# Performance work log

Hardware: AMD Instinct MI355X
Metric: run time of the kernel (lower is better)

The kernel has to match this reference:

```python
import jax, jax.numpy as jnp
import numpy as np

B, N, M = 32, 32, 64          # batch, timesteps, local group length (group_token_length+3)
NL, NG = 192, 768             # n_embd_local, n_embd_global
HL, HG = 6, 12                # n_head_local, n_head_global


def setup_inputs() -> dict:
    key = jax.random.key(0)
    ks = jax.random.split(key, 16)
    def w(k, shape, s=0.02):
        return jax.random.normal(k, shape, jnp.float32) * s
    inp = {}
    inp["xl"] = jax.random.normal(ks[0], (B, N, M, NL), jnp.float32)
    inp["xg"] = jax.random.normal(ks[1], (B, 2 * N, NG), jnp.float32)
    i = 2
    for pre, d in (("l", NL), ("g", NG)):
        inp[f"{pre}_ln1_w"] = jnp.ones((d,), jnp.float32)
        inp[f"{pre}_ln1_b"] = jnp.zeros((d,), jnp.float32)
        inp[f"{pre}_ln2_w"] = jnp.ones((d,), jnp.float32)
        inp[f"{pre}_ln2_b"] = jnp.zeros((d,), jnp.float32)
        for nm in ("q", "k", "v", "o"):
            inp[f"{pre}_w{nm}"] = w(ks[i], (d, d)); i += 1
            inp[f"{pre}_b{nm}"] = jnp.zeros((d,), jnp.float32)
        inp[f"{pre}_w1"] = w(ks[i], (d, 4 * d)); i += 1
        inp[f"{pre}_b1"] = jnp.zeros((4 * d,), jnp.float32)
        inp[f"{pre}_w2"] = w(ks[i], (4 * d, d)); i += 1
        inp[f"{pre}_b2"] = jnp.zeros((d,), jnp.float32)
    inp["d_w"] = w(ks[i], (M * NL, NG))
    inp["d_b"] = jnp.zeros((NG,), jnp.float32)
    return inp


def _ln(x, g, b):
    m = x.mean(-1, keepdims=True)
    v = ((x - m) ** 2).mean(-1, keepdims=True)
    return (x - m) / jnp.sqrt(v + 1e-5) * g + b


def _attn(x, wq, bq, wk, bk, wv, bv, wo, bo, nh, allow):
    # x: [B', L, D]; allow: [L, L] bool (True = attend)
    Bx, L, D = x.shape
    hd = D // nh
    q = (x @ wq + bq).reshape(Bx, L, nh, hd)
    k = (x @ wk + bk).reshape(Bx, L, nh, hd)
    v = (x @ wv + bv).reshape(Bx, L, nh, hd)
    s = jnp.einsum('bihd,bjhd->bhij', q, k) / np.float32(np.sqrt(hd))
    s = jnp.where(allow[None, None], s, -jnp.inf)
    p = jax.nn.softmax(s, axis=-1)
    y = jnp.einsum('bhij,bjhd->bihd', p, v).reshape(Bx, L, D)
    return y @ wo + bo


def _tblock(x, p, nh, allow):
    (ln1w, ln1b, ln2w, ln2b, wq, bq, wk, bk, wv, bv, wo, bo, w1, b1, w2, b2) = p
    x = x + _attn(_ln(x, ln1w, ln1b), wq, bq, wk, bk, wv, bv, wo, bo, nh, allow)
    h = _ln(x, ln2w, ln2b)
    return x + (jax.nn.gelu(h @ w1 + b1, approximate=False) @ w2 + b2)


def reference(xl, xg,
              l_ln1_w, l_ln1_b, l_ln2_w, l_ln2_b,
              l_wq, l_bq, l_wk, l_bk, l_wv, l_bv, l_wo, l_bo,
              l_w1, l_b1, l_w2, l_b2,
              g_ln1_w, g_ln1_b, g_ln2_w, g_ln2_b,
              g_wq, g_bq, g_wk, g_bk, g_wv, g_bv, g_wo, g_bo,
              g_w1, g_b1, g_w2, g_b2,
              d_w, d_b):
    Bx, Nx, Mx, nl = xl.shape
    ng = xg.shape[-1]
    lp = (l_ln1_w, l_ln1_b, l_ln2_w, l_ln2_b, l_wq, l_bq, l_wk, l_bk,
          l_wv, l_bv, l_wo, l_bo, l_w1, l_b1, l_w2, l_b2)
    gp = (g_ln1_w, g_ln1_b, g_ln2_w, g_ln2_b, g_wq, g_bq, g_wk, g_bk,
          g_wv, g_bv, g_wo, g_bo, g_w1, g_b1, g_w2, g_b2)

    # local block: causal attention within each group of M tokens
    allow_l = jnp.tril(jnp.ones((Mx, Mx), bool))
    x = _tblock(xl.reshape(Bx * Nx, Mx, nl), lp, HL, allow_l)
    xl_out = x.reshape(Bx, Nx, Mx, nl)

    # summarize each group into one global token, interleave with xg pairs
    zg = (xl_out.reshape(Bx, Nx, Mx * nl) @ d_w + d_b)[:, :, None, :]  # [B,N,1,ng]
    zg = jnp.concatenate([zg, xg.reshape(Bx, Nx, 2, ng)], axis=2)      # [B,N,3,ng]
    zg = zg.reshape(Bx, 3 * Nx, ng)

    # global mask: tril plus within-triplet upper entries; the global block
    # additionally applies its own causal mask, so combined = causal & custom
    L = 3 * Nx
    idx = jnp.arange(L)
    causal = idx[:, None] >= idx[None, :]
    custom = causal | (idx[:, None] // 3 == idx[None, :] // 3)
    allow_g = causal & custom

    zg = _tblock(zg, gp, HG, allow_g)
    xg_out = zg.reshape(Bx, Nx, 3, ng)[:, :, 1:, :].reshape(Bx, 2 * Nx, ng)
    return (xl_out, xg_out)
```

## Files before the change

kernel.cpp:

```cpp
#include <hip/hip_runtime.h>
#include <hip/hip_bf16.h>


typedef unsigned short ushort;
typedef __bf16 bf16x8 __attribute__((ext_vector_type(8)));
typedef float f32x4 __attribute__((ext_vector_type(4)));

__device__ __forceinline__ ushort f2us(float f) {
  __hip_bfloat16 h = __float2bfloat16(f);
  return *reinterpret_cast<ushort*>(&h);
}
__device__ __forceinline__ float gelu_exact(float v) {
  return 0.5f * v * (1.f + erff(v * 0.70710678118654752f));
}
__device__ __forceinline__ void gload16(const ushort* g, ushort* l) {
  __builtin_amdgcn_global_load_lds(
      (const __attribute__((address_space(1))) void*)g,
      (__attribute__((address_space(3))) void*)l, 16, 0, 0);
}

struct TJobs { const float* s[13]; ushort* d[13]; };

__global__ __launch_bounds__(256)
void transp_all(TJobs J)
{
  static constexpr int NN[13]  = {192,192,192,192,768,192,768,768,768,768,768,3072,768};
  static constexpr int SS[13]  = {192,192,192,192,192,768,12288,768,768,768,768,768,3072};
  static constexpr int RO[13]  = {0,192,384,0,0,0,0,0,768,1536,0,0,0};
  static constexpr int CUM[14] = {0,9,18,27,36,72,108,2412,2556,2700,2844,2988,3564,4140};
  __shared__ float t[64][65];
  int bid = blockIdx.x;
  int j = 0;
  while (bid >= CUM[j + 1]) ++j;
  int tIdx = bid - CUM[j];
  const int N = NN[j], stride = SS[j], rowOff = RO[j];
  const int nx = N >> 6;
  const int n0 = (tIdx % nx) * 64, k0 = (tIdx / nx) * 64;
  const float* W = J.s[j];
  ushort* Wt = J.d[j];
  int c = threadIdx.x & 63, r = threadIdx.x >> 6;
  #pragma unroll
  for (int i = 0; i < 16; ++i) {
    int kr = r + i * 4;
    t[kr][c] = W[(size_t)(k0 + kr) * N + n0 + c];
  }
  __syncthreads();
  #pragma unroll
  for (int i = 0; i < 16; ++i) {
    int nr = r + i * 4;
    Wt[(size_t)(rowOff + n0 + nr) * stride + k0 + c] = f2us(t[c][nr]);
  }
}

__global__ __launch_bounds__(256)
void pack3_kernel(float* dst, const float* a, int na, const float* b, int nb,
                  const float* c, int nc)
{
  int i = blockIdx.x * 256 + threadIdx.x;
  if (i >= na + nb + nc) return;
  dst[i] = (i < na) ? a[i] : (i < na + nb ? b[i - na] : c[i - na - nb]);
}

template<int D>
__global__ __launch_bounds__(256)
void ln_kernel(const float* __restrict__ x, const float* __restrict__ g,
               const float* __restrict__ bb, ushort* __restrict__ out, int rows)
{
  int wave = threadIdx.x >> 6, lane = threadIdx.x & 63;
  int row = blockIdx.x * 4 + wave;
  if (row >= rows) return;
  const float* xr = x + (size_t)row * D;
  constexpr int E = D / 64;
  float vals[E];
  float s = 0.f;
  #pragma unroll
  for (int e = 0; e < E; ++e) { vals[e] = xr[e * 64 + lane]; s += vals[e]; }
  #pragma unroll
  for (int off = 32; off >= 1; off >>= 1) s += __shfl_xor(s, off);
  float m = s * (1.f / D);
  float s2 = 0.f;
  #pragma unroll
  for (int e = 0; e < E; ++e) { float d = vals[e] - m; s2 += d * d; }
  #pragma unroll
  for (int off = 32; off >= 1; off >>= 1) s2 += __shfl_xor(s2, off);
  float rstd = rsqrtf(s2 * (1.f / D) + 1e-5f);
  ushort* orow = out + (size_t)row * D;
  #pragma unroll
  for (int e = 0; e < E; ++e) {
    int c = e * 64 + lane;
    orow[c] = f2us((vals[e] - m) * rstd * g[c] + bb[c]);
  }
}

template<int ACT, int RES, int OUTF, int OUTB, int BIAS>
__global__ __launch_bounds__(256)
void mgemm(const ushort* __restrict__ A, const ushort* __restrict__ Bt,
           const float* __restrict__ bias, const float* __restrict__ resF,
           float* __restrict__ Cf, ushort* __restrict__ Cb,
           int M, int N, int K)
{
  __shared__ __align__(16) ushort Asm[2][128 * 32];
  __shared__ __align__(16) ushort Bsm[2][64 * 32];
  const int tid = threadIdx.x;
  const int wave = tid >> 6, lane = tid & 63;
  const int quad = lane >> 4, lm = lane & 15;
  const int rowBase = blockIdx.y * 128, colBase = blockIdx.x * 64;
  const int wrow = (wave & 1) * 64, wcol = (wave >> 1) * 32;
  const int srow = lane >> 2, skcol = (lane & 3) * 8;
  const int nIter = K >> 5;

  auto stage = [&](int buf, int it) {
    const int k0 = it * 32;
    #pragma unroll
    for (int uu = 0; uu < 3; ++uu) {
      const int u = wave * 3 + uu;
      if (u < 8) {
        const ushort* gp = A + (size_t)(rowBase + u * 16 + srow) * K + k0 + skcol;
        gload16(gp, &Asm[buf][u * 512]);
      } else {
        const int v = u - 8;
        const ushort* gp = Bt + (size_t)(colBase + v * 16 + srow) * K + k0 + skcol;
        gload16(gp, &Bsm[buf][v * 512]);
      }
    }
  };

  f32x4 acc[4][2] = {};
  stage(0, 0);
  if (nIter > 1) stage(1, 1);

  for (int t = 0; t < nIter; ++t) {
    const int cur = t & 1;
    if (t + 1 < nIter) asm volatile("s_waitcnt vmcnt(3)" ::: "memory");
    else               asm volatile("s_waitcnt vmcnt(0)" ::: "memory");
    __builtin_amdgcn_s_barrier();
    bf16x8 af[4], bfr[2];
    #pragma unroll
    for (int r2 = 0; r2 < 4; ++r2)
      af[r2] = *reinterpret_cast<const bf16x8*>(&Asm[cur][(wrow + r2 * 16 + lm) * 32 + quad * 8]);
    #pragma unroll
    for (int c2 = 0; c2 < 2; ++c2)
      bfr[c2] = *reinterpret_cast<const bf16x8*>(&Bsm[cur][(wcol + c2 * 16 + lm) * 32 + quad * 8]);
    asm volatile("s_waitcnt lgkmcnt(0)" ::: "memory");
    __builtin_amdgcn_s_barrier();
    if (t + 2 < nIter) stage(cur, t + 2);
    #pragma unroll
    for (int r2 = 0; r2 < 4; ++r2)
      #pragma unroll
      for (int c2 = 0; c2 < 2; ++c2)
        acc[r2][c2] = __builtin_amdgcn_mfma_f32_16x16x32_bf16(af[r2], bfr[c2], acc[r2][c2], 0, 0, 0);
  }

  #pragma unroll
  for (int r2 = 0; r2 < 4; ++r2) {
    #pragma unroll
    for (int c2 = 0; c2 < 2; ++c2) {
      int col = colBase + wcol + c2 * 16 + lm;
      int row0 = rowBase + wrow + r2 * 16 + quad * 4;
      #pragma unroll
      for (int g = 0; g < 4; ++g) {
        float v = acc[r2][c2][g];
        size_t idx = (size_t)(row0 + g) * N + col;
        if (BIAS) v += bias[col];
        if (ACT == 1) v = gelu_exact(v);
        if (RES) v += resF[idx];
        if (OUTF) Cf[idx] = v;
        if (OUTB) Cb[idx] = f2us(v);
      }
    }
  }
}

template<int ACT, int RES, int OUTF, int OUTB, int BIAS, int SPLITK>
__global__ __launch_bounds__(256)
void mgemm128(const ushort* __restrict__ A, const ushort* __restrict__ Bt,
              const float* __restrict__ bias, const float* __restrict__ resF,
              float* __restrict__ Cf, ushort* __restrict__ Cb,
              int M, int N, int K, int kChunk)
{
  __shared__ __align__(16) ushort Asm[2][128 * 32];
  __shared__ __align__(16) ushort Bsm[2][128 * 32];
  const int tid = threadIdx.x;
  const int wave = tid >> 6, lane = tid & 63;
  const int quad = lane >> 4, lm = lane & 15;
  const int rowBase = blockIdx.y * 128, colBase = blockIdx.x * 128;
  const int wrow = (wave & 1) * 64, wcol = (wave >> 1) * 64;
  const int srow = lane >> 2, skcol = (lane & 3) * 8;

  const int kbeg = SPLITK ? blockIdx.z * kChunk : 0;
  const int nIter = (SPLITK ? kChunk : K) >> 5;

  auto stage = [&](int buf, int it) {
    const int k0 = kbeg + it * 32;
    #pragma unroll
    for (int uu = 0; uu < 4; ++uu) {
      const int u = wave * 4 + uu;
      if (u < 8) {
        const ushort* gp = A + (size_t)(rowBase + u * 16 + srow) * K + k0 + skcol;
        gload16(gp, &Asm[buf][u * 512]);
      } else {
        const int v = u - 8;
        const ushort* gp = Bt + (size_t)(colBase + v * 16 + srow) * K + k0 + skcol;
        gload16(gp, &Bsm[buf][v * 512]);
      }
    }
  };

  f32x4 acc[4][4] = {};
  stage(0, 0);
  if (nIter > 1) stage(1, 1);

  for (int t = 0; t < nIter; ++t) {
    const int cur = t & 1;
    if (t + 1 < nIter) asm volatile("s_waitcnt vmcnt(4)" ::: "memory");
    else               asm volatile("s_waitcnt vmcnt(0)" ::: "memory");
    __builtin_amdgcn_s_barrier();
    bf16x8 af[4], bfr[4];
    #pragma unroll
    for (int r2 = 0; r2 < 4; ++r2)
      af[r2] = *reinterpret_cast<const bf16x8*>(&Asm[cur][(wrow + r2 * 16 + lm) * 32 + quad * 8]);
    #pragma unroll
    for (int c2 = 0; c2 < 4; ++c2)
      bfr[c2] = *reinterpret_cast<const bf16x8*>(&Bsm[cur][(wcol + c2 * 16 + lm) * 32 + quad * 8]);
    asm volatile("s_waitcnt lgkmcnt(0)" ::: "memory");
    __builtin_amdgcn_s_barrier();
    if (t + 2 < nIter) stage(cur, t + 2);
    #pragma unroll
    for (int r2 = 0; r2 < 4; ++r2)
      #pragma unroll
      for (int c2 = 0; c2 < 4; ++c2)
        acc[r2][c2] = __builtin_amdgcn_mfma_f32_16x16x32_bf16(af[r2], bfr[c2], acc[r2][c2], 0, 0, 0);
  }

  const size_t zoff = SPLITK ? (size_t)blockIdx.z * M * N : 0;
  #pragma unroll
  for (int r2 = 0; r2 < 4; ++r2) {
    #pragma unroll
    for (int c2 = 0; c2 < 4; ++c2) {
      int col = colBase + wcol + c2 * 16 + lm;
      int row0 = rowBase + wrow + r2 * 16 + quad * 4;
      #pragma unroll
      for (int g = 0; g < 4; ++g) {
        float v = acc[r2][c2][g];
        size_t idx = (size_t)(row0 + g) * N + col;
        if (BIAS) v += bias[col];
        if (ACT == 1) v = gelu_exact(v);
        if (RES) v += resF[idx];
        if (OUTF) Cf[zoff + idx] = v;
        if (OUTB) Cb[idx] = f2us(v);
      }
    }
  }
}

__global__ __launch_bounds__(256)
void reduce8_kernel(const float* __restrict__ P, const float* __restrict__ db,
                    float* __restrict__ ZG)
{
  int i = blockIdx.x * 256 + threadIdx.x;
  float s = db[i % 768];
  #pragma unroll
  for (int k = 0; k < 8; ++k) s += P[i + k * 786432];
  ZG[i] = s;
}

__global__ __launch_bounds__(256)
void reduce4res_kernel(const float* __restrict__ P, const float* __restrict__ db,
                       const float* __restrict__ res, float* __restrict__ out)
{
  int i = blockIdx.x * 256 + threadIdx.x;
  float s = db[i % 768] + res[i];
  #pragma unroll
  for (int k = 0; k < 4; ++k) s += P[i + k * 2359296];
  out[i] = s;
}

template<int L, int HD, int NW>
__global__ __launch_bounds__(NW * 64)
void fattn(const ushort* __restrict__ QKV, ushort* __restrict__ Yp,
           int nh, int DS, int DY, int offQ, int offK, int offV)
{
  constexpr int PQ = HD + 8;
  constexpr int PV = L + 8;
  constexpr int KS = HD / 32;
  constexpr int NCT = L / 16;
  constexpr int KS2 = L / 32;
  constexpr int NYT = HD / 16;
  constexpr int T = NW * 64;
  __shared__ __align__(16) ushort Ql[L * PQ];
  __shared__ __align__(16) ushort Kl[L * PQ];
  __shared__ __align__(16) ushort Vt[HD * PV];
  __shared__ __align__(16) ushort Ps[L * PV];
  const int tid = threadIdx.x;
  const int b = blockIdx.x / nh, h = blockIdx.x % nh;
  const size_t rowb = (size_t)b * L * DS;
  const int hb = h * HD;
  constexpr int CH = L * HD / 8;
  for (int idx = tid; idx < CH; idx += T) {
    int row = idx / (HD / 8), seg = idx % (HD / 8);
    uint4 q4 = *reinterpret_cast<const uint4*>(&QKV[rowb + (size_t)row * DS + offQ + hb + seg * 8]);
    *reinterpret_cast<uint4*>(&Ql[row * PQ + seg * 8]) = q4;
    uint4 k4 = *reinterpret_cast<const uint4*>(&QKV[rowb + (size_t)row * DS + offK + hb + seg * 8]);
    *reinterpret_cast<uint4*>(&Kl[row * PQ + seg * 8]) = k4;
  }
  for (int idx = tid; idx < L * HD; idx += T) {
    int j = idx / HD, d = idx % HD;
    Vt[d * PV + j] = QKV[rowb + (size_t)j * DS + offV + hb + d];
  }
  __syncthreads();
  const int lane = tid & 63;
  const int quad = lane >> 4, lm = lane & 15;
  const int rt = tid >> 6;
  const float scale = rsqrtf((float)HD);
  bf16x8 af[KS];
  #pragma unroll
  for (int s = 0; s < KS; ++s)
    af[s] = *reinterpret_cast<const bf16x8*>(&Ql[(rt * 16 + lm) * PQ + s * 32 + quad * 8]);
  f32x4 sacc[NCT] = {};
  #pragma unroll
  for (int ct = 0; ct < NCT; ++ct)
    #pragma unroll
    for (int s = 0; s < KS; ++s) {
      bf16x8 bf = *reinterpret_cast<const bf16x8*>(&Kl[(ct * 16 + lm) * PQ + s * 32 + quad * 8]);
      sacc[ct] = __builtin_amdgcn_mfma_f32_16x16x32_bf16(af[s], bf, sacc[ct], 0, 0, 0);
    }
  float inv[4];
  #pragma unroll
  for (int g = 0; g < 4; ++g) {
    const int row = rt * 16 + quad * 4 + g;
    float sv[NCT]; float m = -1e30f;
    #pragma unroll
    for (int ct = 0; ct < NCT; ++ct) {
      int col = ct * 16 + lm;
      float x = sacc[ct][g] * scale;
      sv[ct] = (col <= row) ? x : -1e30f;
      m = fmaxf(m, sv[ct]);
    }
    #pragma unroll
    for (int off = 8; off >= 1; off >>= 1) m = fmaxf(m, __shfl_xor(m, off));
    float l = 0.f;
    #pragma unroll
    for (int ct = 0; ct < NCT; ++ct) {
      float p = __expf(sv[ct] - m);
      l += p;
      Ps[row * PV + ct * 16 + lm] = f2us(p);
    }
    #pragma unroll
    for (int off = 8; off >= 1; off >>= 1) l += __shfl_xor(l, off);
    inv[g] = 1.f / l;
  }
  __syncthreads();
  f32x4 yacc[NYT] = {};
  #pragma unroll
  for (int s = 0; s < KS2; ++s) {
    bf16x8 ap = *reinterpret_cast<const bf16x8*>(&Ps[(rt * 16 + lm) * PV + s * 32 + quad * 8]);
    #pragma unroll
    for (int ct = 0; ct < NYT; ++ct) {
      bf16x8 bv = *reinterpret_cast<const bf16x8*>(&Vt[(ct * 16 + lm) * PV + s * 32 + quad * 8]);
      yacc[ct] = __builtin_amdgcn_mfma_f32_16x16x32_bf16(ap, bv, yacc[ct], 0, 0, 0);
    }
  }
  #pragma unroll
  for (int ct = 0; ct < NYT; ++ct)
    #pragma unroll
    for (int g = 0; g < 4; ++g) {
      int row = rt * 16 + quad * 4 + g;
      int d = ct * 16 + lm;
      Yp[((size_t)b * L + row) * DY + hb + d] = f2us(yacc[ct][g] * inv[g]);
    }
}

__global__ __launch_bounds__(256)
void interleave_kernel(const float* __restrict__ zg, const float* __restrict__ xg,
                       float* __restrict__ z)
{
  int idx = blockIdx.x * 256 + threadIdx.x;
  int c = idx % 768;
  int tok = idx / 768;
  int b = tok / 96, r = tok % 96;
  int n = r / 3, t = r % 3;
  z[idx] = (t == 0) ? zg[((size_t)b * 32 + n) * 768 + c]
                    : xg[((size_t)b * 64 + 2 * n + (t - 1)) * 768 + c];
}

__global__ __launch_bounds__(256)
void gather_kernel(const float* __restrict__ zfin, float* __restrict__ dst)
{
  int idx = blockIdx.x * 256 + threadIdx.x;
  int c = idx % 768;
  int t = (idx / 768) % 64;
  int b = idx / (768 * 64);
  int n = t >> 1, s = t & 1;
  dst[idx] = zfin[((size_t)b * 96 + 3 * n + 1 + s) * 768 + c];
}

extern "C" void kernel_launch(void* const* d_in, const int* in_sizes, int n_in,
                              void* d_out, int out_size, void* d_ws, size_t ws_size,
                              hipStream_t stream) {
  const float* xl = (const float*)d_in[0];
  const float* xg = (const float*)d_in[1];
  const float* l_ln1_w = (const float*)d_in[2];  const float* l_ln1_b = (const float*)d_in[3];
  const float* l_ln2_w = (const float*)d_in[4];  const float* l_ln2_b = (const float*)d_in[5];
  const float* l_wq = (const float*)d_in[6];     const float* l_bq = (const float*)d_in[7];
  const float* l_wk = (const float*)d_in[8];     const float* l_bk = (const float*)d_in[9];
  const float* l_wv = (const float*)d_in[10];    const float* l_bv = (const float*)d_in[11];
  const float* l_wo = (const float*)d_in[12];    const float* l_bo = (const float*)d_in[13];
  const float* l_w1 = (const float*)d_in[14];    const float* l_b1 = (const float*)d_in[15];
  const float* l_w2 = (const float*)d_in[16];    const float* l_b2 = (const float*)d_in[17];
  const float* g_ln1_w = (const float*)d_in[18]; const float* g_ln1_b = (const float*)d_in[19];
  const float* g_ln2_w = (const float*)d_in[20]; const float* g_ln2_b = (const float*)d_in[21];
  const float* g_wq = (const float*)d_in[22];    const float* g_bq = (const float*)d_in[23];
  const float* g_wk = (const float*)d_in[24];    const float* g_bk = (const float*)d_in[25];
  const float* g_wv = (const float*)d_in[26];    const float* g_bv = (const float*)d_in[27];
  const float* g_wo = (const float*)d_in[28];    const float* g_bo = (const float*)d_in[29];
  const float* g_w1 = (const float*)d_in[30];    const float* g_b1 = (const float*)d_in[31];
  const float* g_w2 = (const float*)d_in[32];    const float* g_b2 = (const float*)d_in[33];
  const float* dw   = (const float*)d_in[34];    const float* db   = (const float*)d_in[35];

  float* outL = (float*)d_out;
  float* outG = outL + 12582912;

  char* W = (char*)d_ws;
  ushort* A_bf   = (ushort*)(W + 0);
  ushort* QKVl   = (ushort*)(W + 25165824);
  ushort* HIDl   = (ushort*)(W + 25165824);
  ushort* XLb    = (ushort*)(W + 75497472);
  float*  X1     = (float*)(W + 100663296);
  ushort* wqkv_t = (ushort*)(W + 150994944);
  ushort* wo_t   = (ushort*)(W + 151216128);
  ushort* w1_t   = (ushort*)(W + 151289856);
  ushort* w2_t   = (ushort*)(W + 151584768);
  ushort* wd_t   = (ushort*)(W + 151879680);
  ushort* wgqkv_t= (ushort*)(W + 170754048);
  ushort* wgo_t  = (ushort*)(W + 174292992);
  ushort* wg1_t  = (ushort*)(W + 175472640);
  ushort* wg2_t  = (ushort*)(W + 180191232);
  float*  bqkv_l = (float*)(W + 184909824);
  float*  bqkv_g = (float*)(W + 184912128);
  float*  ZGP  = (float*)(W + 0);
  float*  FC2P = (float*)(W + 0);
  float*  ZG   = (float*)(W + 25165824);
  float*  Z    = (float*)(W + 28311552);
  ushort* LNG  = (ushort*)(W + 37748736);
  ushort* QKVg = (ushort*)(W + 42467328);
  ushort* YG   = (ushort*)(W + 56623104);
  float*  X1G  = (float*)(W + 61341696);
  ushort* HLNG = (ushort*)(W + 70778880);
  ushort* HIDg = (ushort*)(W + 100663296);
  float*  OUTG = (float*)(W + 119537664);

  TJobs tj;
  tj.s[0] = l_wq; tj.s[1] = l_wk; tj.s[2] = l_wv; tj.s[3] = l_wo;
  tj.s[4] = l_w1; tj.s[5] = l_w2; tj.s[6] = dw;
  tj.s[7] = g_wq; tj.s[8] = g_wk; tj.s[9] = g_wv; tj.s[10] = g_wo;
  tj.s[11] = g_w1; tj.s[12] = g_w2;
  tj.d[0] = wqkv_t; tj.d[1] = wqkv_t; tj.d[2] = wqkv_t; tj.d[3] = wo_t;
  tj.d[4] = w1_t; tj.d[5] = w2_t; tj.d[6] = wd_t;
  tj.d[7] = wgqkv_t; tj.d[8] = wgqkv_t; tj.d[9] = wgqkv_t; tj.d[10] = wgo_t;
  tj.d[11] = wg1_t; tj.d[12] = wg2_t;
  transp_all<<<4140, 256, 0, stream>>>(tj);
  pack3_kernel<<<3, 256, 0, stream>>>(bqkv_l, l_bq, 192, l_bk, 192, l_bv, 192);
  pack3_kernel<<<9, 256, 0, stream>>>(bqkv_g, g_bq, 768, g_bk, 768, g_bv, 768);

  ln_kernel<192><<<16384, 256, 0, stream>>>(xl, l_ln1_w, l_ln1_b, A_bf, 65536);
  mgemm<0,0,0,1,1><<<dim3(9,512), 256, 0, stream>>>(A_bf, wqkv_t, bqkv_l, nullptr, nullptr, QKVl, 65536, 576, 192);
  fattn<64,32,4><<<6144, 256, 0, stream>>>(QKVl, A_bf, 6, 576, 192, 0, 192, 384);
  mgemm<0,1,1,0,1><<<dim3(3,512), 256, 0, stream>>>(A_bf, wo_t, l_bo, xl, X1, nullptr, 65536, 192, 192);
  ln_kernel<192><<<16384, 256, 0, stream>>>(X1, l_ln2_w, l_ln2_b, A_bf, 65536);
  for (int h = 0; h < 2; ++h) {
    size_t ro = (size_t)h * 32768 * 192;
    mgemm128<1,0,0,1,1,0><<<dim3(6,256), 256, 0, stream>>>(A_bf + ro, w1_t, l_b1, nullptr, nullptr, HIDl, 32768, 768, 192, 0);
    mgemm<0,1,1,1,1><<<dim3(3,256), 256, 0, stream>>>(HIDl, w2_t, l_b2, X1 + ro, outL + ro, XLb + ro, 32768, 192, 768);
  }
  mgemm128<0,0,1,0,0,1><<<dim3(6,8,8), 256, 0, stream>>>(XLb, wd_t, nullptr, nullptr, ZGP, nullptr, 1024, 768, 12288, 1536);
  reduce8_kernel<<<3072, 256, 0, stream>>>(ZGP, db, ZG);
  interleave_kernel<<<9216, 256, 0, stream>>>(ZG, xg, Z);
  ln_kernel<768><<<768, 256, 0, stream>>>(Z, g_ln1_w, g_ln1_b, LNG, 3072);
  mgemm128<0,0,0,1,1,0><<<dim3(18,24), 256, 0, stream>>>(LNG, wgqkv_t, bqkv_g, nullptr, nullptr, QKVg, 3072, 2304, 768, 0);
  fattn<96,64,6><<<384, 384, 0, stream>>>(QKVg, YG, 12, 2304, 768, 0, 768, 1536);
  mgemm<0,1,1,0,1><<<dim3(12,24), 256, 0, stream>>>(YG, wgo_t, g_bo, Z, X1G, nullptr, 3072, 768, 768);
  ln_kernel<768><<<768, 256, 0, stream>>>(X1G, g_ln2_w, g_ln2_b, HLNG, 3072);
  mgemm128<1,0,0,1,1,0><<<dim3(24,24), 256, 0, stream>>>(HLNG, wg1_t, g_b1, nullptr, nullptr, HIDg, 3072, 3072, 768, 0);
  mgemm128<0,0,1,0,0,1><<<dim3(6,24,4), 256, 0, stream>>>(HIDg, wg2_t, nullptr, nullptr, FC2P, nullptr, 3072, 768, 3072, 768);
  reduce4res_kernel<<<9216, 256, 0, stream>>>(FC2P, g_b2, X1G, OUTG);
  gather_kernel<<<6144, 256, 0, stream>>>(OUTG, outG);
}
```

Before: 660.3 us.

## Fuse local MLP FC1+GELU+FC2 into one kernel keeping hidden in LDS

Replaces the two-pass local MLP (FC1 GEMM writing a bf16 hidden buffer, then FC2 GEMM with residual) with a single kernel. Each block owns 64 rows, computes the hidden activations 64 columns at a time into shared memory, and accumulates FC2 in registers, streaming W1/W2 tiles through registers into LDS. This removes the global write and re-read of the 65536x768 hidden tensor and several launches. In exchange it has lower per-block parallelism (1024 blocks, high register use for acc and A fragments) and frequent syncs per hidden tile.

```diff
diff --git a/kernel.cpp b/kernel.cpp
--- a/kernel.cpp
+++ b/kernel.cpp
@@ -90,6 +90,142 @@
     int c = e * 64 + lane;
     orow[c] = f2us((vals[e] - m) * rstd * g[c] + bb[c]);
   }
+}
+
+__global__ __launch_bounds__(256)
+void fused_mlp(const ushort* __restrict__ A, const ushort* __restrict__ W1t,
+               const ushort* __restrict__ W2t, const float* __restrict__ b1,
+               const float* __restrict__ b2, const float* __restrict__ resF,
+               float* __restrict__ Cf, ushort* __restrict__ Cb)
+{
+  __shared__ __align__(16) ushort W1B[64 * 200];
+  __shared__ __align__(16) ushort W2B[192 * 72];
+  __shared__ __align__(16) ushort Hs[64 * 72];
+  const int tid = threadIdx.x;
+  const int wave = tid >> 6, lane = tid & 63;
+  const int quad = lane >> 4, lm = lane & 15;
+  const int rowBase = blockIdx.x * 64;
+  const int wr  = (wave & 1) * 32;
+  const int wc1 = (wave >> 1) * 32;
+  const int wc2 = (wave >> 1) * 96;
+
+  bf16x8 afr[2][6];
+  #pragma unroll
+  for (int r2 = 0; r2 < 2; ++r2)
+    #pragma unroll
+    for (int kt = 0; kt < 6; ++kt)
+      afr[r2][kt] = *reinterpret_cast<const bf16x8*>(
+          &A[(size_t)(rowBase + wr + r2 * 16 + lm) * 192 + kt * 32 + quad * 8]);
+
+  uint4 rs1[6], rs2[6];
+  #pragma unroll
+  for (int i = 0; i < 6; ++i) {
+    int seg = tid + i * 256, row = seg / 24, kk = (seg % 24) * 8;
+    rs1[i] = *reinterpret_cast<const uint4*>(&W1t[(size_t)row * 192 + kk]);
+  }
+  #pragma unroll
+  for (int i = 0; i < 6; ++i) {
+    int seg = tid + i * 256, row = seg / 24, kk = (seg % 24) * 8;
+    *reinterpret_cast<uint4*>(&W1B[row * 200 + kk]) = rs1[i];
+  }
+  #pragma unroll
+  for (int i = 0; i < 6; ++i) {
+    int seg = tid + i * 256, row = seg / 8, kk = (seg % 8) * 8;
+    rs2[i] = *reinterpret_cast<const uint4*>(&W2t[(size_t)row * 768 + kk]);
+  }
+  __syncthreads();
+
+  f32x4 acc2[2][6] = {};
+  for (int ht = 0; ht < 12; ++ht) {
+    f32x4 acc1[2][2] = {};
+    #pragma unroll
+    for (int kt = 0; kt < 6; ++kt) {
+      bf16x8 bfr[2];
+      #pragma unroll
+      for (int c2 = 0; c2 < 2; ++c2)
+        bfr[c2] = *reinterpret_cast<const bf16x8*>(
+            &W1B[(wc1 + c2 * 16 + lm) * 200 + kt * 32 + quad * 8]);
+      #pragma unroll
+      for (int r2 = 0; r2 < 2; ++r2)
+        #pragma unroll
+        for (int c2 = 0; c2 < 2; ++c2)
+          acc1[r2][c2] = __builtin_amdgcn_mfma_f32_16x16x32_bf16(
+              afr[r2][kt], bfr[c2], acc1[r2][c2], 0, 0, 0);
+    }
+    #pragma unroll
+    for (int r2 = 0; r2 < 2; ++r2)
+      #pragma unroll
+      for (int c2 = 0; c2 < 2; ++c2) {
+        int col = wc1 + c2 * 16 + lm;
+        float bb1 = b1[ht * 64 + col];
+        #pragma unroll
+        for (int g = 0; g < 4; ++g) {
+          int row = wr + r2 * 16 + quad * 4 + g;
+          Hs[row * 72 + col] = f2us(gelu_exact(acc1[r2][c2][g] + bb1));
+        }
+      }
+    #pragma unroll
+    for (int i = 0; i < 6; ++i) {
+      int seg = tid + i * 256, row = seg / 8, kk = (seg % 8) * 8;
+      *reinterpret_cast<uint4*>(&W2B[row * 72 + kk]) = rs2[i];
+    }
+    if (ht + 1 < 12) {
+      #pragma unroll
+      for (int i = 0; i < 6; ++i) {
+        int seg = tid + i * 256, row = seg / 24, kk = (seg % 24) * 8;
+        rs1[i] = *reinterpret_cast<const uint4*>(
+            &W1t[(size_t)((ht + 1) * 64 + row) * 192 + kk]);
+      }
+    }
+    __syncthreads();
+    #pragma unroll
+    for (int s = 0; s < 2; ++s) {
+      bf16x8 ap[2], bp[6];
+      #pragma unroll
+      for (int r2 = 0; r2 < 2; ++r2)
+        ap[r2] = *reinterpret_cast<const bf16x8*>(
+            &Hs[(wr + r2 * 16 + lm) * 72 + s * 32 + quad * 8]);
+      #pragma unroll
+      for (int c2 = 0; c2 < 6; ++c2)
+        bp[c2] = *reinterpret_cast<const bf16x8*>(
+            &W2B[(wc2 + c2 * 16 + lm) * 72 + s * 32 + quad * 8]);
+      #pragma unroll
+      for (int r2 = 0; r2 < 2; ++r2)
+        #pragma unroll
+        for (int c2 = 0; c2 < 6; ++c2)
+          acc2[r2][c2] = __builtin_amdgcn_mfma_f32_16x16x32_bf16(
+              ap[r2], bp[c2], acc2[r2][c2], 0, 0, 0);
+    }
+    if (ht + 1 < 12) {
+      #pragma unroll
+      for (int i = 0; i < 6; ++i) {
+        int seg = tid + i * 256, row = seg / 24, kk = (seg % 24) * 8;
+        *reinterpret_cast<uint4*>(&W1B[row * 200 + kk]) = rs1[i];
+      }
+      #pragma unroll
+      for (int i = 0; i < 6; ++i) {
+        int seg = tid + i * 256, row = seg / 8, kk = (seg % 8) * 8;
+        rs2[i] = *reinterpret_cast<const uint4*>(
+            &W2t[(size_t)row * 768 + (ht + 1) * 64 + kk]);
+      }
+      __syncthreads();
+    }
+  }
+  #pragma unroll
+  for (int r2 = 0; r2 < 2; ++r2)
+    #pragma unroll
+    for (int c2 = 0; c2 < 6; ++c2) {
+      int col = wc2 + c2 * 16 + lm;
+      float bb2 = b2[col];
+      #pragma unroll
+      for (int g = 0; g < 4; ++g) {
+        int row = rowBase + wr + r2 * 16 + quad * 4 + g;
+        size_t idx = (size_t)row * 192 + col;
+        float v = acc2[r2][c2][g] + bb2 + resF[idx];
+        Cf[idx] = v;
+        Cb[idx] = f2us(v);
+      }
+    }
 }
 
 template<int ACT, int RES, int OUTF, int OUTB, int BIAS>
@@ -423,7 +559,6 @@
   char* W = (char*)d_ws;
   ushort* A_bf   = (ushort*)(W + 0);
   ushort* QKVl   = (ushort*)(W + 25165824);
-  ushort* HIDl   = (ushort*)(W + 25165824);
   ushort* XLb    = (ushort*)(W + 75497472);
   float*  X1     = (float*)(W + 100663296);
   ushort* wqkv_t = (ushort*)(W + 150994944);
@@ -467,11 +602,7 @@
   fattn<64,32,4><<<6144, 256, 0, stream>>>(QKVl, A_bf, 6, 576, 192, 0, 192, 384);
   mgemm<0,1,1,0,1><<<dim3(3,512), 256, 0, stream>>>(A_bf, wo_t, l_bo, xl, X1, nullptr, 65536, 192, 192);
   ln_kernel<192><<<16384, 256, 0, stream>>>(X1, l_ln2_w, l_ln2_b, A_bf, 65536);
-  for (int h = 0; h < 2; ++h) {
-    size_t ro = (size_t)h * 32768 * 192;
-    mgemm128<1,0,0,1,1,0><<<dim3(6,256), 256, 0, stream>>>(A_bf + ro, w1_t, l_b1, nullptr, nullptr, HIDl, 32768, 768, 192, 0);
-    mgemm<0,1,1,1,1><<<dim3(3,256), 256, 0, stream>>>(HIDl, w2_t, l_b2, X1 + ro, outL + ro, XLb + ro, 32768, 192, 768);
-  }
+  fused_mlp<<<1024, 256, 0, stream>>>(A_bf, w1_t, w2_t, l_b1, l_b2, X1, outL, XLb);
   mgemm128<0,0,1,0,0,1><<<dim3(6,8,8), 256, 0, stream>>>(XLb, wd_t, nullptr, nullptr, ZGP, nullptr, 1024, 768, 12288, 1536);
   reduce8_kernel<<<3072, 256, 0, stream>>>(ZGP, db, ZG);
   interleave_kernel<<<9216, 256, 0, stream>>>(ZG, xg, Z);
```

New measurement: 735.4 us. 11.4% more time.
